# Optimization experiments

Measured on AMD Instinct MI355X. Metric: run time of the kernel, lower is better.

Reference implementation:

```python
import jax, jax.numpy as jnp
import numpy as np

PAD_Y = 16
PAD_X = 16


def setup_inputs() -> dict:
    key = jax.random.key(0)
    k1, k2, k3, k4 = jax.random.split(key, 4)
    B, NLAM, H, W = 4, 96, 256, 256
    KS = 15
    cube = jax.random.normal(k1, (B, NLAM, H, W), dtype=jnp.float32)
    # per-(ksequence, wavelength) dispersion shifts in pixels (a few px)
    dx = 3.0 * jax.random.normal(k2, (4, NLAM), dtype=jnp.float32)
    dy = 3.0 * jax.random.normal(k3, (4, NLAM), dtype=jnp.float32)
    psf = jax.random.uniform(k4, (KS, KS), dtype=jnp.float32)
    psf = psf / psf.sum()  # normalised PSF as in the original
    return {"cube": cube, "dx": dx, "dy": dy, "psf_kernel": psf}


def _forward(cube, dx, dy, psf_kernel):
    B, n_lam, H, W = cube.shape
    H_out, W_out = H + 2 * PAD_Y, W + 2 * PAD_X
    padded = jnp.pad(cube, ((0, 0), (0, 0), (PAD_Y, PAD_Y), (PAD_X, PAD_X)))
    yy, xx = jnp.meshgrid(jnp.arange(H_out, dtype=cube.dtype),
                          jnp.arange(W_out, dtype=cube.dtype), indexing="ij")

    def shift_one(img_b, d_x, d_y):
        # img_b: (B, H_out, W_out); output[y,x] = input[y-dy, x-dx], bilinear,
        # zeros outside (matches grid_sample padding_mode='zeros', align_corners=True)
        coords = jnp.stack([yy - d_y, xx - d_x])  # (2, H_out, W_out)
        return jax.vmap(lambda im: jax.scipy.ndimage.map_coordinates(
            im, coords, order=1, mode="constant", cval=0.0))(img_b)

    def per_k(dxk, dyk):
        # vmap over wavelengths -> (n_lam, B, H_out, W_out); accumulate over lambda
        shifted = jax.vmap(shift_one, in_axes=(1, 0, 0))(padded, dxk, dyk)
        return shifted.sum(0)  # (B, H_out, W_out)

    acc = jax.vmap(per_k)(dx, dy)            # (4, B, H_out, W_out)
    acc = jnp.transpose(acc, (1, 0, 2, 3))   # (B, 4, H_out, W_out)

    # PSF conv (same kernel every channel); conv is linear so conv(sum) == sum(conv)
    ks = psf_kernel.shape[-1]
    p = ks // 2
    x = acc.reshape(B * 4, 1, H_out, W_out)
    kern = psf_kernel.reshape(1, 1, ks, ks)
    out = jax.lax.conv_general_dilated(
        x, kern, window_strides=(1, 1), padding=[(p, p), (p, p)],
        dimension_numbers=("NCHW", "OIHW", "NCHW"))
    return out.reshape(B, 4, H_out, W_out)


def reference(cube, dx, dy, psf_kernel):
    return _forward(cube, dx, dy, psf_kernel)
```

## Files before the change

### kernel.cpp

```cpp
#include <hip/hip_runtime.h>

#define BB 4
#define NLAM 96
#define HH 256
#define WW 256
#define HO 288
#define WO 288
#define NK 4
#define KS 15
#define PADK 7

#define ACC_N ((size_t)BB * NK * HO * WO)

#define SP 104
#define NQ 7
#define TILE_Q (NQ * 256)

typedef float f4a __attribute__((ext_vector_type(4)));
typedef float f8v __attribute__((ext_vector_type(8), aligned(16)));

__global__ __launch_bounds__(384) void params_k(const float* __restrict__ dx,
                                                const float* __restrict__ dy,
                                                float4* __restrict__ pw,
                                                int2* __restrict__ po,
                                                int4* __restrict__ gmm,
                                                float* __restrict__ zp) {
    __shared__ int sox[384], soy[384];
    const int i = threadIdx.x;
    if (i < 32) zp[i] = 0.0f;
    const float sx = -dx[i] - 16.0f;
    const float sy = -dy[i] - 16.0f;
    const float fx = floorf(sx), fy = floorf(sy);
    const int ox = (int)fx, oy = (int)fy;
    po[i] = make_int2(ox, oy);
    pw[i] = make_float4(1.0f - (sx - fx), sx - fx, 1.0f - (sy - fy), sy - fy);
    sox[i] = ox; soy[i] = oy;
    __syncthreads();
    if (i < 64) {
        int mnx = sox[i], mxx = mnx, mny = soy[i], mxy = mny;
        for (int j = i + 64; j < 384; j += 64) {
            mnx = min(mnx, sox[j]); mxx = max(mxx, sox[j]);
            mny = min(mny, soy[j]); mxy = max(mxy, soy[j]);
        }
        for (int m = 32; m; m >>= 1) {
            mnx = min(mnx, __shfl_xor(mnx, m, 64));
            mxx = max(mxx, __shfl_xor(mxx, m, 64));
            mny = min(mny, __shfl_xor(mny, m, 64));
            mxy = max(mxy, __shfl_xor(mxy, m, 64));
        }
        if (i == 0) *gmm = make_int4(mnx, mxx, mny, mxy);
    }
}

#define HORW(P)                                                          \
    {                                                                    \
        f4a h0  = {vb0[P], vb0[(P)+1], vb0[(P)+2], vb0[(P)+3]};          \
        f4a h0s = {vb0[(P)+1], vb0[(P)+2], vb0[(P)+3], vb0[(P)+4]};      \
        f4a h1  = {vb1[P], vb1[(P)+1], vb1[(P)+2], vb1[(P)+3]};          \
        f4a h1s = {vb1[(P)+1], vb1[(P)+2], vb1[(P)+3], vb1[(P)+4]};      \
        a[k][0] += w.x * h0 + w.y * h0s;                                 \
        a[k][1] += w.x * h1 + w.y * h1s;                                 \
    }

__global__ __launch_bounds__(256, 2) void shift_accum(
        const float* __restrict__ cube,
        const float4* __restrict__ pw,
        const int2* __restrict__ po,
        const int4* __restrict__ gmm,
        const float* __restrict__ zp,
        float* __restrict__ part,
        int S, int chunk) {
    __shared__ __align__(16) float tile[TILE_Q * 4 + 8];
    const int zc  = blockIdx.z;
    const int b   = zc / S;
    const int c   = zc - b * S;
    const int tx0 = blockIdx.x * 64;
    const int ty0 = blockIdx.y * 32;
    const int tx  = threadIdx.x, ty = threadIdx.y;
    const int x   = tx0 + tx * 4;
    const int y   = ty0 + ty * 2;
    const int tid = ty * 16 + tx;
    const float* __restrict__ cb = cube + (size_t)b * NLAM * HH * WW;

    const int4 mm = *gmm;
    const int spanX = mm.y - mm.x;
    const int spanY = mm.w - mm.z;
    const bool lds_ok = (spanX <= 32) && (spanY <= 31);

    f4a a[NK][2];
#pragma unroll
    for (int k = 0; k < NK; ++k) { a[k][0] = (f4a)0.f; a[k][1] = (f4a)0.f; }

    const int l0 = min(NLAM, c * chunk);
    const int l1 = min(NLAM, l0 + chunk);

    if (lds_ok) {
        const int row0 = ty0 + mm.z;
        const int col0 = (tx0 + mm.x) & ~3;
        const int R    = spanY + 34;
        const int Rq   = R * 26;
        const int dx0  = tx0 - col0;
        const int tb0  = (ty * 2 - mm.z) * SP + tx * 4 + dx0;
        const int ldsq0 = tid & 192;
        const char* zpc = (const char*)zp;

        int goffB[NQ];
        int fm = 0;
        int pf = 0;
#pragma unroll
        for (int s = 0; s < NQ; ++s) {
            const int q  = tid + s * 256;
            const bool inR = q < Rq;
            const int r  = q / 26;
            const int qi = q - r * 26;
            const int gy = row0 + r;
            const int gc = col0 + qi * 4;
            const bool rowOK = (unsigned)gy < (unsigned)HH;
            const bool fullQ = inR && rowOK && gc >= 0 && gc <= WW - 4;
            const bool partQ = inR && rowOK && !fullQ && (gc + 3 >= 0) && (gc < WW);
            goffB[s] = (gy * WW + gc) * 4;
            if (fullQ) fm |= 1 << s;
            if (partQ) pf |= 1 << s;
        }

        for (int lam = l0; lam < l1; ++lam) {
            const char* __restrict__ ib = (const char*)(cb + lam * (HH * WW));
#pragma unroll
            for (int s = 0; s < NQ; ++s) {
                if (s * 256 < Rq) {
                    const char* src = ((fm >> s) & 1) ? (ib + goffB[s]) : zpc;
                    __builtin_amdgcn_global_load_lds(
                        (const __attribute__((address_space(1))) unsigned int*)src,
                        (__attribute__((address_space(3))) unsigned int*)
                            (tile + (s * 256 + ldsq0) * 4),
                        16, 0, 0);
                }
            }
            if (pf) {
                asm volatile("s_waitcnt vmcnt(0)" ::: "memory");
#pragma unroll
                for (int s = 0; s < NQ; ++s) {
                    if (pf & (1 << s)) {
                        const int q  = tid + s * 256;
                        const int r  = q / 26;
                        const int qi = q - r * 26;
                        const int gy = row0 + r;
                        const int gc = col0 + qi * 4;
                        const float* rp = (const float*)ib + gy * WW;
                        const int la = r * SP + qi * 4;
#pragma unroll
                        for (int e = 0; e < 4; ++e)
                            tile[la + e] = ((unsigned)(gc + e) < (unsigned)WW)
                                               ? rp[gc + e] : 0.0f;
                    }
                }
            }
            __syncthreads();
#pragma unroll
            for (int k = 0; k < NK; ++k) {
                const int2 o = po[k * NLAM + lam];
                const float4 w = pw[k * NLAM + lam];
                const int bidx = tb0 + o.y * SP + o.x;
                const int p = __builtin_amdgcn_readfirstlane(bidx & 3);
                const float* ta = tile + (bidx & ~3);
                const f8v R0 = *(const f8v*)ta;
                const f8v R1 = *(const f8v*)(ta + SP);
                const f8v R2 = *(const f8v*)(ta + 2 * SP);
                const f8v vb0 = w.z * R0 + w.w * R1;
                const f8v vb1 = w.z * R1 + w.w * R2;
                switch (p) {
                    case 0:  HORW(0); break;
                    case 1:  HORW(1); break;
                    case 2:  HORW(2); break;
                    default: HORW(3); break;
                }
            }
            __syncthreads();
        }
    } else {
        for (int lam = l0; lam < l1; ++lam) {
            const float* __restrict__ img = cb + lam * (HH * WW);
#pragma unroll
            for (int k = 0; k < NK; ++k) {
                const int i_ = k * NLAM + lam;
                const int2 o = po[i_]; const float4 w = pw[i_];
#pragma unroll
                for (int j = 0; j < 2; ++j) {
                    const int iy = y + j + o.y;
                    const int ix = x + o.x;
                    const int cy0 = min(max(iy, 0), HH - 1);
                    const int cy1 = min(max(iy + 1, 0), HH - 1);
                    const float my0 = ((unsigned)iy       < (unsigned)HH) ? w.z : 0.0f;
                    const float my1 = ((unsigned)(iy + 1) < (unsigned)HH) ? w.w : 0.0f;
                    const float* r0p = img + cy0 * WW;
                    const float* r1p = img + cy1 * WW;
                    float rb[5];
#pragma unroll
                    for (int cc = 0; cc < 5; ++cc) {
                        const int cx = min(max(ix + cc, 0), WW - 1);
                        const float m = ((unsigned)(ix + cc) < (unsigned)WW) ? 1.0f : 0.0f;
                        rb[cc] = m * (my0 * r0p[cx] + my1 * r1p[cx]);
                    }
                    f4a d;
                    d.x = w.x * rb[0] + w.y * rb[1];
                    d.y = w.x * rb[1] + w.y * rb[2];
                    d.z = w.x * rb[2] + w.y * rb[3];
                    d.w = w.x * rb[3] + w.y * rb[4];
                    a[k][j] += d;
                }
            }
        }
    }

    if (x < WO) {
        const size_t hw = (size_t)HO * WO;
        float* pa = part + (size_t)c * ACC_N + ((size_t)(b * NK) * HO + y) * WO + x;
#pragma unroll
        for (int k = 0; k < NK; ++k) {
            *(f4a*)(pa + (size_t)k * hw)      = a[k][0];
            *(f4a*)(pa + (size_t)k * hw + WO) = a[k][1];
        }
    }
}

#define CPX 112
#define CROWS 30
#define CTILE_N (CROWS * CPX)
#define NQC 5

template <int S>
__global__ __launch_bounds__(192) void conv_psf(const float* __restrict__ part,
                                                const float* __restrict__ psf,
                                                float* __restrict__ out) {
    __shared__ __align__(16) float tilec[CTILE_N + 16];
    __shared__ __align__(16) float spsf[KS][16];
    const int bk  = blockIdx.z;
    const int gx0 = blockIdx.x * 96 - 8;
    const int gy0 = blockIdx.y * 16 - PADK;
    const float* __restrict__ ap = part + (size_t)bk * HO * WO;

    const int tid = threadIdx.y * 24 + threadIdx.x;
    for (int i = tid; i < KS * 16; i += 192) {
        const int r = i >> 4, cc2 = i & 15;
        spsf[r][cc2] = (cc2 < KS) ? psf[r * KS + cc2] : 0.0f;
    }

    int goffB[NQC], laddr[NQC];
    f4a cmask[NQC];
#pragma unroll
    for (int s = 0; s < NQC; ++s) {
        const int q  = tid + s * 192;
        const bool inR = q < CROWS * 28;
        const int r  = q / 28;
        const int qi = q - r * 28;
        const int gy = gy0 + r;
        const int gx = gx0 + qi * 4;
        const bool rowOK = (unsigned)gy < (unsigned)HO;
        const int gyc = min(max(gy, 0), HO - 1);
        goffB[s] = (gyc * WO + gx) * 4;
        laddr[s] = inR ? (r * CPX + qi * 4) : CTILE_N;
        f4a m;
#pragma unroll
        for (int e = 0; e < 4; ++e)
            m[e] = (inR && rowOK && (unsigned)(gx + e) < (unsigned)WO) ? 1.0f : 0.0f;
        cmask[s] = m;
    }

#pragma unroll
    for (int s = 0; s < NQC; ++s) {
        const char* base = (const char*)ap + goffB[s];
        f4a acc = (f4a)0.f;
#pragma unroll
        for (int cc = 0; cc < S; ++cc)
            acc += *(const f4a*)(base + (size_t)cc * (ACC_N * 4));
        acc *= cmask[s];
        *(f4a*)(tilec + laddr[s]) = acc;
    }
    __syncthreads();

    const int x0 = threadIdx.x * 4;
    const int y0 = threadIdx.y * 2;
    f4a o0 = (f4a)0.f, o1 = (f4a)0.f;
    f4a prev0, prev1, prev2, prev3;

#pragma unroll
    for (int rr = 0; rr < 16; ++rr) {
        const float* rp = &tilec[(y0 + rr) * CPX + x0];
        float row[20];
#pragma unroll
        for (int q = 0; q < 5; ++q) {
            f4a v = *(const f4a*)(rp + 4 * q);
            row[4 * q]     = v.x; row[4 * q + 1] = v.y;
            row[4 * q + 2] = v.z; row[4 * q + 3] = v.w;
        }

        f4a c0, c1, c2, c3;
        if (rr < 15) {
            c0 = *(const f4a*)&spsf[rr][0];
            c1 = *(const f4a*)&spsf[rr][4];
            c2 = *(const f4a*)&spsf[rr][8];
            c3 = *(const f4a*)&spsf[rr][12];
        }
        if (rr < 15) {
#pragma unroll
            for (int kx = 0; kx < KS; ++kx) {
                const float wv = (kx < 4) ? c0[kx] : (kx < 8) ? c1[kx - 4]
                               : (kx < 12) ? c2[kx - 8] : c3[kx - 12];
                f4a rv = {row[kx + 1], row[kx + 2], row[kx + 3], row[kx + 4]};
                o0 += wv * rv;
            }
        }
        if (rr >= 1) {
#pragma unroll
            for (int kx = 0; kx < KS; ++kx) {
                const float wv = (kx < 4) ? prev0[kx] : (kx < 8) ? prev1[kx - 4]
                               : (kx < 12) ? prev2[kx - 8] : prev3[kx - 12];
                f4a rv = {row[kx + 1], row[kx + 2], row[kx + 3], row[kx + 4]};
                o1 += wv * rv;
            }
        }
        prev0 = c0; prev1 = c1; prev2 = c2; prev3 = c3;
    }

    const int xo = blockIdx.x * 96 + x0;
    const int yo = blockIdx.y * 16 + y0;
    float* op = out + ((size_t)bk * HO + yo) * WO + xo;
    *(f4a*)op        = o0;
    *(f4a*)(op + WO) = o1;
}

extern "C" void kernel_launch(void* const* d_in, const int* in_sizes, int n_in,
                              void* d_out, int out_size, void* d_ws, size_t ws_size,
                              hipStream_t stream) {
    const float* cube = (const float*)d_in[0];
    const float* dx   = (const float*)d_in[1];
    const float* dy   = (const float*)d_in[2];
    const float* psf  = (const float*)d_in[3];
    float* out = (float*)d_out;

    const size_t ACCB   = ACC_N * sizeof(float);
    const size_t tables = 384 * sizeof(float4) + 384 * sizeof(int2) + sizeof(int4);

    int S = 1;
    for (int cand : {12, 8, 6, 4, 3, 2}) {
        if (ws_size >= 128 + (size_t)cand * ACCB + tables + 4096) { S = cand; break; }
    }
    const int chunk = (NLAM + S - 1) / S;

    float* zp   = (float*)d_ws;
    float* part = (float*)((char*)d_ws + 128);
    char*  tb   = (char*)part + (size_t)S * ACCB;
    float4* pw  = (float4*)tb;
    int2*   po  = (int2*)(tb + 384 * sizeof(float4));
    int4*   gmm = (int4*)(tb + 384 * sizeof(float4) + 384 * sizeof(int2));

    params_k<<<1, 384, 0, stream>>>(dx, dy, pw, po, gmm, zp);

    dim3 b1(16, 16);
    dim3 g1((WO + 63) / 64, HO / 32, BB * S);
    shift_accum<<<g1, b1, 0, stream>>>(cube, pw, po, gmm, zp, part, S, chunk);

    dim3 b2(24, 8);
    dim3 g2(WO / 96, HO / 16, BB * NK);
    switch (S) {
        case 12: conv_psf<12><<<g2, b2, 0, stream>>>(part, psf, out); break;
        case 8:  conv_psf<8><<<g2, b2, 0, stream>>>(part, psf, out); break;
        case 6:  conv_psf<6><<<g2, b2, 0, stream>>>(part, psf, out); break;
        case 4:  conv_psf<4><<<g2, b2, 0, stream>>>(part, psf, out); break;
        case 3:  conv_psf<3><<<g2, b2, 0, stream>>>(part, psf, out); break;
        case 2:  conv_psf<2><<<g2, b2, 0, stream>>>(part, psf, out); break;
        default: conv_psf<1><<<g2, b2, 0, stream>>>(part, psf, out); break;
    }
}
```

Baseline: 219.9 us.

## Double-buffer the LDS tile to prefetch the next wavelength during compute

The shared tile now has two buffers. The direct global-to-LDS loads for wavelength lam+1 are issued before the bilinear accumulation for wavelength lam, and only the current stage's loads are waited for (vmcnt(7)). The goal is to hide global load latency behind the per-wavelength arithmetic and drop one full barrier per iteration in favour of raw s_barrier with explicit waitcnts. In exchange, LDS use per block doubles, which may limit occupancy. All seven staging loads are now issued unconditionally, so extra zero-page loads can occur when the tile needs fewer rows.

```diff
diff --git a/kernel.cpp b/kernel.cpp
--- a/kernel.cpp
+++ b/kernel.cpp
@@ -15,6 +15,7 @@
 #define SP 104
 #define NQ 7
 #define TILE_Q (NQ * 256)
+#define TILE_F (TILE_Q * 4)
 
 typedef float f4a __attribute__((ext_vector_type(4)));
 typedef float f8v __attribute__((ext_vector_type(8), aligned(16)));
@@ -62,6 +63,19 @@
         a[k][1] += w.x * h1 + w.y * h1s;                                 \
     }
 
+#define STAGE_TO(DST, IB)                                                     \
+    {                                                                         \
+        _Pragma("unroll")                                                     \
+        for (int s = 0; s < NQ; ++s) {                                        \
+            const char* src = ((fm >> s) & 1) ? ((IB) + goffB[s]) : zpc;      \
+            __builtin_amdgcn_global_load_lds(                                 \
+                (const __attribute__((address_space(1))) unsigned int*)src,   \
+                (__attribute__((address_space(3))) unsigned int*)             \
+                    ((DST) + (s * 256 + ldsq0) * 4),                          \
+                16, 0, 0);                                                    \
+        }                                                                     \
+    }
+
 __global__ __launch_bounds__(256, 2) void shift_accum(
         const float* __restrict__ cube,
         const float4* __restrict__ pw,
@@ -70,7 +84,7 @@
         const float* __restrict__ zp,
         float* __restrict__ part,
         int S, int chunk) {
-    __shared__ __align__(16) float tile[TILE_Q * 4 + 8];
+    __shared__ __align__(16) float tile[2 * TILE_F + 8];
     const int zc  = blockIdx.z;
     const int b   = zc / S;
     const int c   = zc - b * S;
@@ -97,12 +111,12 @@
     if (lds_ok) {
         const int row0 = ty0 + mm.z;
         const int col0 = (tx0 + mm.x) & ~3;
-        const int R    = spanY + 34;
-        const int Rq   = R * 26;
+        const int Rq   = (spanY + 34) * 26;
         const int dx0  = tx0 - col0;
         const int tb0  = (ty * 2 - mm.z) * SP + tx * 4 + dx0;
         const int ldsq0 = tid & 192;
         const char* zpc = (const char*)zp;
+        (void)Rq;
 
         int goffB[NQ];
         int fm = 0;
@@ -123,21 +137,25 @@
             if (partQ) pf |= 1 << s;
         }
 
+        float* bufC = tile;
+        float* bufN = tile + TILE_F;
+
+        {
+            const char* ib0 = (const char*)(cb + l0 * (HH * WW));
+            STAGE_TO(bufC, ib0)
+        }
+
         for (int lam = l0; lam < l1; ++lam) {
             const char* __restrict__ ib = (const char*)(cb + lam * (HH * WW));
-#pragma unroll
-            for (int s = 0; s < NQ; ++s) {
-                if (s * 256 < Rq) {
-                    const char* src = ((fm >> s) & 1) ? (ib + goffB[s]) : zpc;
-                    __builtin_amdgcn_global_load_lds(
-                        (const __attribute__((address_space(1))) unsigned int*)src,
-                        (__attribute__((address_space(3))) unsigned int*)
-                            (tile + (s * 256 + ldsq0) * 4),
-                        16, 0, 0);
-                }
+            const bool hasNext = (lam + 1 < l1);
+            if (hasNext) {
+                const char* ibn = (const char*)(cb + (lam + 1) * (HH * WW));
+                STAGE_TO(bufN, ibn)
+                asm volatile("s_waitcnt vmcnt(7)" ::: "memory");
+            } else {
+                asm volatile("s_waitcnt vmcnt(0)" ::: "memory");
             }
             if (pf) {
-                asm volatile("s_waitcnt vmcnt(0)" ::: "memory");
 #pragma unroll
                 for (int s = 0; s < NQ; ++s) {
                     if (pf & (1 << s)) {
@@ -147,22 +165,24 @@
                         const int gy = row0 + r;
                         const int gc = col0 + qi * 4;
                         const float* rp = (const float*)ib + gy * WW;
-                        const int la = r * SP + qi * 4;
+                        float* la = bufC + r * SP + qi * 4;
 #pragma unroll
                         for (int e = 0; e < 4; ++e)
-                            tile[la + e] = ((unsigned)(gc + e) < (unsigned)WW)
-                                               ? rp[gc + e] : 0.0f;
+                            la[e] = ((unsigned)(gc + e) < (unsigned)WW)
+                                        ? rp[gc + e] : 0.0f;
                     }
                 }
-            }
-            __syncthreads();
+                asm volatile("s_waitcnt lgkmcnt(0)" ::: "memory");
+            }
+            __builtin_amdgcn_s_barrier();
+            __builtin_amdgcn_sched_barrier(0);
 #pragma unroll
             for (int k = 0; k < NK; ++k) {
                 const int2 o = po[k * NLAM + lam];
                 const float4 w = pw[k * NLAM + lam];
                 const int bidx = tb0 + o.y * SP + o.x;
                 const int p = __builtin_amdgcn_readfirstlane(bidx & 3);
-                const float* ta = tile + (bidx & ~3);
+                const float* ta = bufC + (bidx & ~3);
                 const f8v R0 = *(const f8v*)ta;
                 const f8v R1 = *(const f8v*)(ta + SP);
                 const f8v R2 = *(const f8v*)(ta + 2 * SP);
@@ -175,7 +195,12 @@
                     default: HORW(3); break;
                 }
             }
-            __syncthreads();
+            if (hasNext) {
+                asm volatile("s_waitcnt lgkmcnt(0)" ::: "memory");
+                __builtin_amdgcn_s_barrier();
+                __builtin_amdgcn_sched_barrier(0);
+            }
+            float* t = bufC; bufC = bufN; bufN = t;
         }
     } else {
         for (int lam = l0; lam < l1; ++lam) {
```

Measured after the change: 257.6 us. 17.2% more time.

## Fuse shift-parameter computation into accumulate kernel and cap lambda splits at six

Applied to the files above, without the earlier changes.

Removes the separate params_k launch. Each shift_accum block now computes floor offsets and bilinear weights inline from dx/dy, and computes the per-chunk min/max offset bounds locally with a wavefront reduction. The zero page is cleared with hipMemsetAsync, and the candidate split counts drop to at most 6, which lowers the partial-buffer traffic the conv kernel must sum. In exchange, every block repeats the parameter arithmetic, and each block is more likely to take the LDS path because its bounds cover only its own lambda chunk.

```diff
diff --git a/kernel.cpp b/kernel.cpp
--- a/kernel.cpp
+++ b/kernel.cpp
@@ -19,61 +19,28 @@
 typedef float f4a __attribute__((ext_vector_type(4)));
 typedef float f8v __attribute__((ext_vector_type(8), aligned(16)));
 
-__global__ __launch_bounds__(384) void params_k(const float* __restrict__ dx,
-                                                const float* __restrict__ dy,
-                                                float4* __restrict__ pw,
-                                                int2* __restrict__ po,
-                                                int4* __restrict__ gmm,
-                                                float* __restrict__ zp) {
-    __shared__ int sox[384], soy[384];
-    const int i = threadIdx.x;
-    if (i < 32) zp[i] = 0.0f;
-    const float sx = -dx[i] - 16.0f;
-    const float sy = -dy[i] - 16.0f;
-    const float fx = floorf(sx), fy = floorf(sy);
-    const int ox = (int)fx, oy = (int)fy;
-    po[i] = make_int2(ox, oy);
-    pw[i] = make_float4(1.0f - (sx - fx), sx - fx, 1.0f - (sy - fy), sy - fy);
-    sox[i] = ox; soy[i] = oy;
-    __syncthreads();
-    if (i < 64) {
-        int mnx = sox[i], mxx = mnx, mny = soy[i], mxy = mny;
-        for (int j = i + 64; j < 384; j += 64) {
-            mnx = min(mnx, sox[j]); mxx = max(mxx, sox[j]);
-            mny = min(mny, soy[j]); mxy = max(mxy, soy[j]);
-        }
-        for (int m = 32; m; m >>= 1) {
-            mnx = min(mnx, __shfl_xor(mnx, m, 64));
-            mxx = max(mxx, __shfl_xor(mxx, m, 64));
-            mny = min(mny, __shfl_xor(mny, m, 64));
-            mxy = max(mxy, __shfl_xor(mxy, m, 64));
-        }
-        if (i == 0) *gmm = make_int4(mnx, mxx, mny, mxy);
-    }
-}
-
 #define HORW(P)                                                          \
     {                                                                    \
         f4a h0  = {vb0[P], vb0[(P)+1], vb0[(P)+2], vb0[(P)+3]};          \
         f4a h0s = {vb0[(P)+1], vb0[(P)+2], vb0[(P)+3], vb0[(P)+4]};      \
         f4a h1  = {vb1[P], vb1[(P)+1], vb1[(P)+2], vb1[(P)+3]};          \
         f4a h1s = {vb1[(P)+1], vb1[(P)+2], vb1[(P)+3], vb1[(P)+4]};      \
-        a[k][0] += w.x * h0 + w.y * h0s;                                 \
-        a[k][1] += w.x * h1 + w.y * h1s;                                 \
+        a[k][0] += wx0 * h0 + wx1 * h0s;                                 \
+        a[k][1] += wx0 * h1 + wx1 * h1s;                                 \
     }
 
 __global__ __launch_bounds__(256, 2) void shift_accum(
         const float* __restrict__ cube,
-        const float4* __restrict__ pw,
-        const int2* __restrict__ po,
-        const int4* __restrict__ gmm,
+        const float* __restrict__ dxg,
+        const float* __restrict__ dyg,
         const float* __restrict__ zp,
         float* __restrict__ part,
-        int S, int chunk) {
+        int chunk) {
     __shared__ __align__(16) float tile[TILE_Q * 4 + 8];
+    __shared__ int4 smm;
     const int zc  = blockIdx.z;
-    const int b   = zc / S;
-    const int c   = zc - b * S;
+    const int b   = zc & (BB - 1);
+    const int c   = zc >> 2;
     const int tx0 = blockIdx.x * 64;
     const int ty0 = blockIdx.y * 32;
     const int tx  = threadIdx.x, ty = threadIdx.y;
@@ -82,7 +49,31 @@
     const int tid = ty * 16 + tx;
     const float* __restrict__ cb = cube + (size_t)b * NLAM * HH * WW;
 
-    const int4 mm = *gmm;
+    const int l0 = min(NLAM, c * chunk);
+    const int l1 = min(NLAM, l0 + chunk);
+
+    if (tid < 64) {
+        const int k  = tid >> 4;
+        int mnx = 0x7fffffff, mxx = -0x7fffffff, mny = 0x7fffffff, mxy = -0x7fffffff;
+        for (int lam = l0 + (tid & 15); lam < l1; lam += 16) {
+            const int i = k * NLAM + lam;
+            const float sx = -dxg[i] - 16.0f;
+            const float sy = -dyg[i] - 16.0f;
+            const int ox = (int)floorf(sx);
+            const int oy = (int)floorf(sy);
+            mnx = min(mnx, ox); mxx = max(mxx, ox);
+            mny = min(mny, oy); mxy = max(mxy, oy);
+        }
+        for (int m = 32; m; m >>= 1) {
+            mnx = min(mnx, __shfl_xor(mnx, m, 64));
+            mxx = max(mxx, __shfl_xor(mxx, m, 64));
+            mny = min(mny, __shfl_xor(mny, m, 64));
+            mxy = max(mxy, __shfl_xor(mxy, m, 64));
+        }
+        if (tid == 0) smm = make_int4(mnx, mxx, mny, mxy);
+    }
+    __syncthreads();
+    const int4 mm = smm;
     const int spanX = mm.y - mm.x;
     const int spanY = mm.w - mm.z;
     const bool lds_ok = (spanX <= 32) && (spanY <= 31);
@@ -90,9 +81,6 @@
     f4a a[NK][2];
 #pragma unroll
     for (int k = 0; k < NK; ++k) { a[k][0] = (f4a)0.f; a[k][1] = (f4a)0.f; }
-
-    const int l0 = min(NLAM, c * chunk);
-    const int l1 = min(NLAM, l0 + chunk);
 
     if (lds_ok) {
         const int row0 = ty0 + mm.z;
@@ -158,16 +146,21 @@
             __syncthreads();
 #pragma unroll
             for (int k = 0; k < NK; ++k) {
-                const int2 o = po[k * NLAM + lam];
-                const float4 w = pw[k * NLAM + lam];
-                const int bidx = tb0 + o.y * SP + o.x;
+                const int i_ = k * NLAM + lam;
+                const float sx = -dxg[i_] - 16.0f;
+                const float sy = -dyg[i_] - 16.0f;
+                const float fx = floorf(sx), fy = floorf(sy);
+                const int ox = (int)fx, oy = (int)fy;
+                const float wx1 = sx - fx, wy1 = sy - fy;
+                const float wx0 = 1.0f - wx1, wy0 = 1.0f - wy1;
+                const int bidx = tb0 + oy * SP + ox;
                 const int p = __builtin_amdgcn_readfirstlane(bidx & 3);
                 const float* ta = tile + (bidx & ~3);
                 const f8v R0 = *(const f8v*)ta;
                 const f8v R1 = *(const f8v*)(ta + SP);
                 const f8v R2 = *(const f8v*)(ta + 2 * SP);
-                const f8v vb0 = w.z * R0 + w.w * R1;
-                const f8v vb1 = w.z * R1 + w.w * R2;
+                const f8v vb0 = wy0 * R0 + wy1 * R1;
+                const f8v vb1 = wy0 * R1 + wy1 * R2;
                 switch (p) {
                     case 0:  HORW(0); break;
                     case 1:  HORW(1); break;
@@ -183,15 +176,20 @@
 #pragma unroll
             for (int k = 0; k < NK; ++k) {
                 const int i_ = k * NLAM + lam;
-                const int2 o = po[i_]; const float4 w = pw[i_];
+                const float sx = -dxg[i_] - 16.0f;
+                const float sy = -dyg[i_] - 16.0f;
+                const float fx = floorf(sx), fy = floorf(sy);
+                const int oxv = (int)fx, oyv = (int)fy;
+                const float wx1 = sx - fx, wy1 = sy - fy;
+                const float wx0 = 1.0f - wx1, wy0 = 1.0f - wy1;
 #pragma unroll
                 for (int j = 0; j < 2; ++j) {
-                    const int iy = y + j + o.y;
-                    const int ix = x + o.x;
+                    const int iy = y + j + oyv;
+                    const int ix = x + oxv;
                     const int cy0 = min(max(iy, 0), HH - 1);
                     const int cy1 = min(max(iy + 1, 0), HH - 1);
-                    const float my0 = ((unsigned)iy       < (unsigned)HH) ? w.z : 0.0f;
-                    const float my1 = ((unsigned)(iy + 1) < (unsigned)HH) ? w.w : 0.0f;
+                    const float my0 = ((unsigned)iy       < (unsigned)HH) ? wy0 : 0.0f;
+                    const float my1 = ((unsigned)(iy + 1) < (unsigned)HH) ? wy1 : 0.0f;
                     const float* r0p = img + cy0 * WW;
                     const float* r1p = img + cy1 * WW;
                     float rb[5];
@@ -202,10 +200,10 @@
                         rb[cc] = m * (my0 * r0p[cx] + my1 * r1p[cx]);
                     }
                     f4a d;
-                    d.x = w.x * rb[0] + w.y * rb[1];
-                    d.y = w.x * rb[1] + w.y * rb[2];
-                    d.z = w.x * rb[2] + w.y * rb[3];
-                    d.w = w.x * rb[3] + w.y * rb[4];
+                    d.x = wx0 * rb[0] + wx1 * rb[1];
+                    d.y = wx0 * rb[1] + wx1 * rb[2];
+                    d.z = wx0 * rb[2] + wx1 * rb[3];
+                    d.w = wx0 * rb[3] + wx1 * rb[4];
                     a[k][j] += d;
                 }
             }
@@ -245,8 +243,6 @@
         spsf[r][cc2] = (cc2 < KS) ? psf[r * KS + cc2] : 0.0f;
     }
 
-    int goffB[NQC], laddr[NQC];
-    f4a cmask[NQC];
 #pragma unroll
     for (int s = 0; s < NQC; ++s) {
         const int q  = tid + s * 192;
@@ -257,24 +253,18 @@
         const int gx = gx0 + qi * 4;
         const bool rowOK = (unsigned)gy < (unsigned)HO;
         const int gyc = min(max(gy, 0), HO - 1);
-        goffB[s] = (gyc * WO + gx) * 4;
-        laddr[s] = inR ? (r * CPX + qi * 4) : CTILE_N;
+        const int goffB = (gyc * WO + gx) * 4;
+        const int laddr = inR ? (r * CPX + qi * 4) : CTILE_N;
         f4a m;
 #pragma unroll
         for (int e = 0; e < 4; ++e)
             m[e] = (inR && rowOK && (unsigned)(gx + e) < (unsigned)WO) ? 1.0f : 0.0f;
-        cmask[s] = m;
-    }
-
-#pragma unroll
-    for (int s = 0; s < NQC; ++s) {
-        const char* base = (const char*)ap + goffB[s];
+        const char* base = (const char*)ap + goffB;
         f4a acc = (f4a)0.f;
 #pragma unroll
         for (int cc = 0; cc < S; ++cc)
             acc += *(const f4a*)(base + (size_t)cc * (ACC_N * 4));
-        acc *= cmask[s];
-        *(f4a*)(tilec + laddr[s]) = acc;
+        *(f4a*)(tilec + laddr) = acc * m;
     }
     __syncthreads();
 
@@ -338,33 +328,26 @@
     const float* psf  = (const float*)d_in[3];
     float* out = (float*)d_out;
 
-    const size_t ACCB   = ACC_N * sizeof(float);
-    const size_t tables = 384 * sizeof(float4) + 384 * sizeof(int2) + sizeof(int4);
+    const size_t ACCB = ACC_N * sizeof(float);
 
     int S = 1;
-    for (int cand : {12, 8, 6, 4, 3, 2}) {
-        if (ws_size >= 128 + (size_t)cand * ACCB + tables + 4096) { S = cand; break; }
+    for (int cand : {6, 4, 3, 2}) {
+        if (ws_size >= 128 + (size_t)cand * ACCB + 4096) { S = cand; break; }
     }
     const int chunk = (NLAM + S - 1) / S;
 
     float* zp   = (float*)d_ws;
     float* part = (float*)((char*)d_ws + 128);
-    char*  tb   = (char*)part + (size_t)S * ACCB;
-    float4* pw  = (float4*)tb;
-    int2*   po  = (int2*)(tb + 384 * sizeof(float4));
-    int4*   gmm = (int4*)(tb + 384 * sizeof(float4) + 384 * sizeof(int2));
-
-    params_k<<<1, 384, 0, stream>>>(dx, dy, pw, po, gmm, zp);
+
+    hipMemsetAsync(d_ws, 0, 128, stream);
 
     dim3 b1(16, 16);
-    dim3 g1((WO + 63) / 64, HO / 32, BB * S);
-    shift_accum<<<g1, b1, 0, stream>>>(cube, pw, po, gmm, zp, part, S, chunk);
+    dim3 g1((WO + 63) / 64, HO / 32, S * BB);
+    shift_accum<<<g1, b1, 0, stream>>>(cube, dx, dy, zp, part, chunk);
 
     dim3 b2(24, 8);
     dim3 g2(WO / 96, HO / 16, BB * NK);
     switch (S) {
-        case 12: conv_psf<12><<<g2, b2, 0, stream>>>(part, psf, out); break;
-        case 8:  conv_psf<8><<<g2, b2, 0, stream>>>(part, psf, out); break;
         case 6:  conv_psf<6><<<g2, b2, 0, stream>>>(part, psf, out); break;
         case 4:  conv_psf<4><<<g2, b2, 0, stream>>>(part, psf, out); break;
         case 3:  conv_psf<3><<<g2, b2, 0, stream>>>(part, psf, out); break;
```

New measurement: 247.6 us. 12.6% more time.
